# Optimization experiments

Hardware: AMD Instinct MI355X
Metric: run time of the kernel (lower is better)

The kernel has to match this reference:

```python
import jax, jax.numpy as jnp
import numpy as np

CHUNK = 128  # chunk size for the chunked causal linear-attention scan
EPS = 1e-6


def _feature_map(x):
    # elu(x) + 1, matching torch.nn.functional.elu (alpha=1)
    return jax.nn.elu(x) + 1.0


def _causal_linear(Q, K, V):
    """Chunked causal linear attention.

    Q, K: [N, H, L, D], V: [N, H, L, Dv] (float32).
    Computes out[l] = Q[l] @ sum_{s<=l} K[s]^T V[s] without materializing
    the O(L*D*Dv) cumulative outer-product tensor.
    """
    N, H, L, D = Q.shape
    Dv = V.shape[-1]
    C = L // CHUNK
    # [C, N, H, T, D]
    qc = jnp.moveaxis(Q.reshape(N, H, C, CHUNK, D), 2, 0)
    kc = jnp.moveaxis(K.reshape(N, H, C, CHUNK, D), 2, 0)
    vc = jnp.moveaxis(V.reshape(N, H, C, CHUNK, Dv), 2, 0)
    tri = jnp.tril(jnp.ones((CHUNK, CHUNK), dtype=Q.dtype))  # causal mask within chunk

    def step(S, qkv):
        q, k, v = qkv  # [N, H, T, D], [N, H, T, D], [N, H, T, Dv]
        attn = jnp.einsum('nhtd,nhsd->nhts', q, k) * tri
        out = jnp.einsum('nhts,nhse->nhte', attn, v) \
            + jnp.einsum('nhtd,nhde->nhte', q, S)
        S = S + jnp.einsum('nhsd,nhse->nhde', k, v)
        return S, out

    S0 = jnp.zeros((N, H, D, Dv), dtype=Q.dtype)
    _, outs = jax.lax.scan(step, S0, (qc, kc, vc))  # outs: [C, N, H, T, Dv]
    return jnp.moveaxis(outs, 0, 2).reshape(N, H, L, Dv)


def setup_inputs() -> dict:
    key = jax.random.key(0)
    kq, kk, kv = jax.random.split(key, 3)
    shape = (4, 8192, 8, 64)  # [N, L, H, D]
    return {
        'queries': jax.random.normal(kq, shape, dtype=jnp.float32),
        'keys': jax.random.normal(kk, shape, dtype=jnp.float32),
        'values': jax.random.normal(kv, shape, dtype=jnp.float32),
    }


def reference(queries, keys, values):
    dtype = queries.dtype
    Q = _feature_map(queries)  # [N, L, H, D]
    K = _feature_map(keys)
    # normalizer: Z = 1 / (Q . cumsum_l(K) + eps), shape [N, L, H]
    Z = 1.0 / (jnp.einsum('nlhi,nlhi->nlh', Q, jnp.cumsum(K, axis=1)) + EPS)
    # numerator computed in float32 per original causal_linear
    Qf = jnp.transpose(Q, (0, 2, 1, 3)).astype(jnp.float32)
    Kf = jnp.transpose(K, (0, 2, 1, 3)).astype(jnp.float32)
    Vf = jnp.transpose(values, (0, 2, 1, 3)).astype(jnp.float32)
    Vn = _causal_linear(Qf, Kf, Vf)  # [N, H, L, Dv]
    Vn = jnp.transpose(Vn, (0, 2, 1, 3)).astype(dtype)  # [N, L, H, Dv]
    return Vn * Z[:, :, :, None]
```

## Files before the change

kernel.cpp:

```cpp
#include <hip/hip_runtime.h>
#include <math.h>

#define N_    4
#define L_    8192
#define H_    8
#define NH_   32
#define CHK   64
#define NSEG  32
#define SEGC  4
#define NC_   128
#define ROWF  512
#define EPSF  1e-6f

typedef __attribute__((ext_vector_type(8))) short bf16x8;
typedef __attribute__((ext_vector_type(4))) float f32x4;
typedef __attribute__((ext_vector_type(4))) unsigned short us4;

__device__ __forceinline__ float fmap(float x) { return x > 0.f ? x + 1.f : __expf(x); }

__device__ __forceinline__ unsigned short f2bf(float x) {
  unsigned u = __float_as_uint(x);
  u += 0x7FFFu + ((u >> 16) & 1u);
  return (unsigned short)(u >> 16);
}
__device__ __forceinline__ float bf2f(unsigned short u) {
  return __uint_as_float(((unsigned)u) << 16);
}

__device__ __forceinline__ int sidx(int row, int col) {
  return row * 64 + (col ^ ((row & 7) << 3));
}

__device__ __forceinline__ f32x4 MFMA(bf16x8 a, bf16x8 b, f32x4 c) {
  return __builtin_amdgcn_mfma_f32_16x16x32_bf16(a, b, c, 0, 0, 0);
}

__global__ __launch_bounds__(256) void k_seg_sums(const float* __restrict__ keys,
                                                  const float* __restrict__ values,
                                                  float* __restrict__ SegTot,
                                                  unsigned short* __restrict__ IntraPre,
                                                  float* __restrict__ KsegTot,
                                                  float* __restrict__ KintraPre) {
  __shared__ unsigned short Kt[64 * 64];
  __shared__ unsigned short Vt[64 * 64];
  __shared__ float kacc[64];
  const int bid = blockIdx.x;
  const int nh = bid / NSEG, seg = bid % NSEG;
  const int n = nh / H_, h = nh % H_;
  const int tid = threadIdx.x;
  const int lane = tid & 63;
  const int wv = tid >> 6;
  const int lane15 = lane & 15, lg = lane >> 4;
  const int arow = wv * 16 + lane15;

  if (tid < 64) kacc[tid] = 0.f;
  __syncthreads();

  f32x4 sAcc[4];
#pragma unroll
  for (int nt = 0; nt < 4; ++nt) sAcc[nt] = (f32x4){0.f, 0.f, 0.f, 0.f};

  for (int ci = 0; ci < SEGC; ++ci) {
    const int c = seg * SEGC + ci;
    const int l0 = c * CHK;
    float kpart = 0.f;
    {
      const int d = tid & 63, sg = tid >> 6;
      const size_t gbase = ((size_t)(n * L_ + l0)) * ROWF + h * 64 + d;
      for (int rep = 0; rep < 4; ++rep) {
        const int s0 = (sg * 4 + rep) * 4;
        us4 wk, wvv;
#pragma unroll
        for (int j = 0; j < 4; ++j) {
          const size_t g = gbase + (size_t)(s0 + j) * ROWF;
          const float kf = fmap(keys[g]);
          kpart += kf;
          wk[j] = f2bf(kf);
          wvv[j] = f2bf(values[g]);
        }
        *(us4*)&Kt[sidx(d, s0)] = wk;
        *(us4*)&Vt[sidx(d, s0)] = wvv;
      }
    }
    {
      unsigned short* ip = IntraPre + ((size_t)nh * NC_ + c) * 4096;
#pragma unroll
      for (int nt = 0; nt < 4; ++nt)
#pragma unroll
        for (int r = 0; r < 4; ++r)
          ip[(size_t)(wv * 16 + lg * 4 + r) * 64 + nt * 16 + lane15] = f2bf(sAcc[nt][r]);
    }
    if (tid < 64) KintraPre[((size_t)nh * NC_ + c) * 64 + tid] = kacc[tid];
    __syncthreads();

    atomicAdd(&kacc[tid & 63], kpart);

    const bf16x8 av0 = *(const bf16x8*)&Vt[sidx(arow, lg * 8)];
    const bf16x8 av1 = *(const bf16x8*)&Vt[sidx(arow, (lg + 4) * 8)];
#pragma unroll
    for (int nt = 0; nt < 4; ++nt) {
      const int brow = nt * 16 + lane15;
      sAcc[nt] = MFMA(av0, *(const bf16x8*)&Kt[sidx(brow, lg * 8)], sAcc[nt]);
      sAcc[nt] = MFMA(av1, *(const bf16x8*)&Kt[sidx(brow, (lg + 4) * 8)], sAcc[nt]);
    }
    __syncthreads();
  }

  float* Sg = SegTot + (size_t)bid * 4096;
#pragma unroll
  for (int nt = 0; nt < 4; ++nt)
#pragma unroll
    for (int r = 0; r < 4; ++r)
      Sg[(size_t)(wv * 16 + lg * 4 + r) * 64 + nt * 16 + lane15] = sAcc[nt][r];
  if (tid < 64) KsegTot[(size_t)bid * 64 + tid] = kacc[tid];
}

__global__ __launch_bounds__(256) void k_prefix(float* __restrict__ SegTot, float* __restrict__ KsegTot) {
  const int tid = threadIdx.x;
  if (blockIdx.x < 512) {
    const int gid = blockIdx.x * 256 + tid;
    const int nh = gid >> 12, de = gid & 4095;
    float* p = SegTot + (size_t)nh * NSEG * 4096 + de;
    float run = 0.f;
    for (int s = 0; s < NSEG; ++s) {
      const float x = p[(size_t)s * 4096];
      p[(size_t)s * 4096] = run;
      run += x;
    }
  } else {
    const int gid = (blockIdx.x - 512) * 256 + tid;
    const int nh = gid >> 6, d = gid & 63;
    float* p = KsegTot + (size_t)nh * NSEG * 64 + d;
    float run = 0.f;
    for (int s = 0; s < NSEG; ++s) {
      const float x = p[s * 64];
      p[s * 64] = run;
      run += x;
    }
  }
}

__global__ __launch_bounds__(256, 6) void k_output(const float* __restrict__ queries,
                                                   const float* __restrict__ keys,
                                                   const float* __restrict__ values,
                                                   const float* __restrict__ SegPre,
                                                   const unsigned short* __restrict__ IntraPre,
                                                   const float* __restrict__ KsegPre,
                                                   const float* __restrict__ KintraPre,
                                                   float* __restrict__ out) {
  __shared__ unsigned short Ks[64 * 64];
  __shared__ unsigned short Vt[64 * 64];
  __shared__ unsigned short St[64 * 64];
  __shared__ float kpre[64];
  __shared__ float zinv[64];

  const int bid = blockIdx.x;
  const int nh = bid / NC_, c = bid % NC_;
  const int seg = c / SEGC;
  const int n = nh / H_, h = nh % H_;
  const int tid = threadIdx.x;
  const int lane = tid & 63;
  const int wv = tid >> 6;
  const int lane15 = lane & 15, lg = lane >> 4;
  const int t0w = wv * 16;
  const int trow = t0w + lane15;
  const int l0 = c * CHK;

  {
    const int r0 = tid >> 4, c4 = (tid & 15) * 4;
    for (int rep = 0; rep < 4; ++rep) {
      const int row = r0 + rep * 16;
      const size_t g = ((size_t)(n * L_ + l0 + row)) * ROWF + h * 64 + c4;
      const float4 k = *(const float4*)&keys[g];
      us4 uk;
      uk[0] = f2bf(fmap(k.x)); uk[1] = f2bf(fmap(k.y));
      uk[2] = f2bf(fmap(k.z)); uk[3] = f2bf(fmap(k.w));
      *(us4*)&Ks[sidx(row, c4)] = uk;
    }
  }
  {
    const int d = tid & 63, sg = tid >> 6;
    const size_t gbase = ((size_t)(n * L_ + l0)) * ROWF + h * 64 + d;
    for (int rep = 0; rep < 4; ++rep) {
      const int s0 = (sg * 4 + rep) * 4;
      us4 w;
#pragma unroll
      for (int j = 0; j < 4; ++j) w[j] = f2bf(values[gbase + (size_t)(s0 + j) * ROWF]);
      *(us4*)&Vt[sidx(d, s0)] = w;
    }
  }
  {
    const float* sp = SegPre + ((size_t)nh * NSEG + seg) * 4096;
    const unsigned short* ip = IntraPre + ((size_t)nh * NC_ + c) * 4096;
    const int r0 = tid >> 4, c4 = (tid & 15) * 4;
    for (int rep = 0; rep < 4; ++rep) {
      const int row = r0 + rep * 16;
      const float4 s4 = *(const float4*)&sp[row * 64 + c4];
      const us4 i4 = *(const us4*)&ip[row * 64 + c4];
      us4 w;
      w[0] = f2bf(s4.x + bf2f(i4[0]));
      w[1] = f2bf(s4.y + bf2f(i4[1]));
      w[2] = f2bf(s4.z + bf2f(i4[2]));
      w[3] = f2bf(s4.w + bf2f(i4[3]));
      *(us4*)&St[sidx(row, c4)] = w;
    }
  }
  if (tid < 64)
    kpre[tid] = KsegPre[((size_t)nh * NSEG + seg) * 64 + tid] +
                KintraPre[((size_t)nh * NC_ + c) * 64 + tid];
  bf16x8 qf0, qf1;
  {
    const size_t qg = ((size_t)(n * L_ + l0 + trow)) * ROWF + h * 64;
    const float4 a = *(const float4*)&queries[qg + lg * 8];
    const float4 b = *(const float4*)&queries[qg + lg * 8 + 4];
    const float4 cc = *(const float4*)&queries[qg + 32 + lg * 8];
    const float4 d4 = *(const float4*)&queries[qg + 32 + lg * 8 + 4];
    qf0[0] = (short)f2bf(fmap(a.x)); qf0[1] = (short)f2bf(fmap(a.y));
    qf0[2] = (short)f2bf(fmap(a.z)); qf0[3] = (short)f2bf(fmap(a.w));
    qf0[4] = (short)f2bf(fmap(b.x)); qf0[5] = (short)f2bf(fmap(b.y));
    qf0[6] = (short)f2bf(fmap(b.z)); qf0[7] = (short)f2bf(fmap(b.w));
    qf1[0] = (short)f2bf(fmap(cc.x)); qf1[1] = (short)f2bf(fmap(cc.y));
    qf1[2] = (short)f2bf(fmap(cc.z)); qf1[3] = (short)f2bf(fmap(cc.w));
    qf1[4] = (short)f2bf(fmap(d4.x)); qf1[5] = (short)f2bf(fmap(d4.y));
    qf1[6] = (short)f2bf(fmap(d4.z)); qf1[7] = (short)f2bf(fmap(d4.w));
  }
  __syncthreads();

  f32x4 aT[4];
#pragma unroll
  for (int nt = 0; nt < 4; ++nt) {
    const int srow = nt * 16 + lane15;
    f32x4 a = {0.f, 0.f, 0.f, 0.f};
    a = MFMA(*(const bf16x8*)&Ks[sidx(srow, lg * 8)], qf0, a);
    a = MFMA(*(const bf16x8*)&Ks[sidx(srow, (lg + 4) * 8)], qf1, a);
    aT[nt] = a;
  }
  float zp = 0.f;
#pragma unroll
  for (int j = 0; j < 8; ++j) zp += bf2f((unsigned short)qf0[j]) * kpre[lg * 8 + j];
#pragma unroll
  for (int j = 0; j < 8; ++j) zp += bf2f((unsigned short)qf1[j]) * kpre[32 + lg * 8 + j];

  __syncthreads();

  float rs = 0.f;
#pragma unroll
  for (int nt = 0; nt < 4; ++nt) {
    us4 w;
#pragma unroll
    for (int r = 0; r < 4; ++r) {
      const int s = nt * 16 + lg * 4 + r;
      const float v = (s <= trow) ? aT[nt][r] : 0.f;
      rs += v;
      w[r] = f2bf(v);
    }
    *(us4*)&Ks[sidx(trow, nt * 16 + lg * 4)] = w;
  }
  float den = rs + zp;
  den += __shfl_xor(den, 16);
  den += __shfl_xor(den, 32);
  const float zv = 1.f / (den + EPSF);
  if (lg == 0) zinv[trow] = zv;

  const bf16x8 af0 = *(const bf16x8*)&Ks[sidx(trow, lg * 8)];
  const bf16x8 af1 = *(const bf16x8*)&Ks[sidx(trow, 32 + lg * 8)];
#pragma unroll
  for (int nt = 0; nt < 4; ++nt) {
    const int brow = nt * 16 + lane15;
    f32x4 o = {0.f, 0.f, 0.f, 0.f};
    o = MFMA(af0, *(const bf16x8*)&Vt[sidx(brow, lg * 8)], o);
    o = MFMA(af1, *(const bf16x8*)&Vt[sidx(brow, (lg + 4) * 8)], o);
    o = MFMA(qf0, *(const bf16x8*)&St[sidx(brow, lg * 8)], o);
    o = MFMA(qf1, *(const bf16x8*)&St[sidx(brow, (lg + 4) * 8)], o);
    const int e = nt * 16 + lane15;
#pragma unroll
    for (int r = 0; r < 4; ++r) {
      const int t = t0w + lg * 4 + r;
      out[((size_t)(n * L_ + l0 + t)) * ROWF + h * 64 + e] = o[r] * zinv[t];
    }
  }
}

extern "C" void kernel_launch(void* const* d_in, const int* in_sizes, int n_in,
                              void* d_out, int out_size, void* d_ws, size_t ws_size,
                              hipStream_t stream) {
  const float* queries = (const float*)d_in[0];
  const float* keys    = (const float*)d_in[1];
  const float* values  = (const float*)d_in[2];
  float* out = (float*)d_out;

  const size_t segtot_e = (size_t)NH_ * NSEG * 4096;
  const size_t intra_e  = (size_t)NH_ * NC_ * 4096;
  const size_t kseg_e   = (size_t)NH_ * NSEG * 64;
  const size_t kintra_e = (size_t)NH_ * NC_ * 64;
  const size_t need = segtot_e * 4 + intra_e * 2 + kseg_e * 4 + kintra_e * 4;
  if (ws_size < need) return;
  float* SegTot = (float*)d_ws;
  unsigned short* IntraPre = (unsigned short*)(SegTot + segtot_e);
  float* KsegTot = (float*)(IntraPre + intra_e);
  float* KintraPre = KsegTot + kseg_e;

  hipLaunchKernelGGL(k_seg_sums, dim3(NH_ * NSEG), dim3(256), 0, stream,
                     keys, values, SegTot, IntraPre, KsegTot, KintraPre);
  hipLaunchKernelGGL(k_prefix, dim3(512 + 8), dim3(256), 0, stream, SegTot, KsegTot);
  hipLaunchKernelGGL(k_output, dim3(NH_ * NC_), dim3(256), 0, stream,
                     queries, keys, values, SegTot, IntraPre, KsegTot, KintraPre, out);
}
```

Measured before the change: 101.2 us.

## Vectorize global loads/stores and transpose MFMA outputs for contiguous writes

Global reads of keys and values now use float4 loads along the feature dimension, with the transpose into LDS done by scattered 16-bit stores. Column sums of keys are reduced with wave shuffles before a few LDS atomics, replacing one atomic per thread. MFMA operands are swapped so each lane holds four contiguous output columns, which allows float4 stores of the output and SegTot and us4 stores of IntraPre, and removes the zinv shared array. The output kernel also remaps block indices in a strided order to spread work across heads and chunks. The scalar LDS transpose writes may cause bank conflicts.

```diff
diff --git a/kernel.cpp b/kernel.cpp
--- a/kernel.cpp
+++ b/kernel.cpp
@@ -60,58 +60,71 @@
 #pragma unroll
   for (int nt = 0; nt < 4; ++nt) sAcc[nt] = (f32x4){0.f, 0.f, 0.f, 0.f};
 
+  const int d4 = tid >> 4, sg = tid & 15;
+
   for (int ci = 0; ci < SEGC; ++ci) {
     const int c = seg * SEGC + ci;
     const int l0 = c * CHK;
-    float kpart = 0.f;
-    {
-      const int d = tid & 63, sg = tid >> 6;
-      const size_t gbase = ((size_t)(n * L_ + l0)) * ROWF + h * 64 + d;
-      for (int rep = 0; rep < 4; ++rep) {
-        const int s0 = (sg * 4 + rep) * 4;
-        us4 wk, wvv;
-#pragma unroll
-        for (int j = 0; j < 4; ++j) {
-          const size_t g = gbase + (size_t)(s0 + j) * ROWF;
-          const float kf = fmap(keys[g]);
-          kpart += kf;
-          wk[j] = f2bf(kf);
-          wvv[j] = f2bf(values[g]);
-        }
-        *(us4*)&Kt[sidx(d, s0)] = wk;
-        *(us4*)&Vt[sidx(d, s0)] = wvv;
+    float kp[4] = {0.f, 0.f, 0.f, 0.f};
+#pragma unroll
+    for (int j = 0; j < 4; ++j) {
+      const int s = sg * 4 + j;
+      const size_t g = ((size_t)(n * L_ + l0 + s)) * ROWF + h * 64 + d4 * 4;
+      const float4 k4 = *(const float4*)&keys[g];
+      const float4 v4 = *(const float4*)&values[g];
+      const float kf[4] = {fmap(k4.x), fmap(k4.y), fmap(k4.z), fmap(k4.w)};
+      const float vf[4] = {v4.x, v4.y, v4.z, v4.w};
+#pragma unroll
+      for (int m = 0; m < 4; ++m) {
+        kp[m] += kf[m];
+        Kt[sidx(d4 * 4 + m, s)] = f2bf(kf[m]);
+        Vt[sidx(d4 * 4 + m, s)] = f2bf(vf[m]);
       }
     }
     {
       unsigned short* ip = IntraPre + ((size_t)nh * NC_ + c) * 4096;
-#pragma unroll
-      for (int nt = 0; nt < 4; ++nt)
-#pragma unroll
-        for (int r = 0; r < 4; ++r)
-          ip[(size_t)(wv * 16 + lg * 4 + r) * 64 + nt * 16 + lane15] = f2bf(sAcc[nt][r]);
+      const int e = wv * 16 + lane15;
+#pragma unroll
+      for (int nt = 0; nt < 4; ++nt) {
+        us4 w;
+#pragma unroll
+        for (int r = 0; r < 4; ++r) w[r] = f2bf(sAcc[nt][r]);
+        *(us4*)&ip[(size_t)e * 64 + nt * 16 + lg * 4] = w;
+      }
     }
     if (tid < 64) KintraPre[((size_t)nh * NC_ + c) * 64 + tid] = kacc[tid];
     __syncthreads();
 
-    atomicAdd(&kacc[tid & 63], kpart);
+#pragma unroll
+    for (int m = 0; m < 4; ++m) {
+      float v = kp[m];
+      v += __shfl_xor(v, 1);
+      v += __shfl_xor(v, 2);
+      v += __shfl_xor(v, 4);
+      v += __shfl_xor(v, 8);
+      if (lane15 == 0) atomicAdd(&kacc[d4 * 4 + m], v);
+    }
 
     const bf16x8 av0 = *(const bf16x8*)&Vt[sidx(arow, lg * 8)];
     const bf16x8 av1 = *(const bf16x8*)&Vt[sidx(arow, (lg + 4) * 8)];
 #pragma unroll
     for (int nt = 0; nt < 4; ++nt) {
       const int brow = nt * 16 + lane15;
-      sAcc[nt] = MFMA(av0, *(const bf16x8*)&Kt[sidx(brow, lg * 8)], sAcc[nt]);
-      sAcc[nt] = MFMA(av1, *(const bf16x8*)&Kt[sidx(brow, (lg + 4) * 8)], sAcc[nt]);
+      sAcc[nt] = MFMA(*(const bf16x8*)&Kt[sidx(brow, lg * 8)], av0, sAcc[nt]);
+      sAcc[nt] = MFMA(*(const bf16x8*)&Kt[sidx(brow, (lg + 4) * 8)], av1, sAcc[nt]);
     }
     __syncthreads();
   }
 
-  float* Sg = SegTot + (size_t)bid * 4096;
-#pragma unroll
-  for (int nt = 0; nt < 4; ++nt)
-#pragma unroll
-    for (int r = 0; r < 4; ++r)
-      Sg[(size_t)(wv * 16 + lg * 4 + r) * 64 + nt * 16 + lane15] = sAcc[nt][r];
+  {
+    float* Sg = SegTot + (size_t)bid * 4096;
+    const int e = wv * 16 + lane15;
+#pragma unroll
+    for (int nt = 0; nt < 4; ++nt) {
+      const float4 w = make_float4(sAcc[nt][0], sAcc[nt][1], sAcc[nt][2], sAcc[nt][3]);
+      *(float4*)&Sg[(size_t)e * 64 + nt * 16 + lg * 4] = w;
+    }
+  }
   if (tid < 64) KsegTot[(size_t)bid * 64 + tid] = kacc[tid];
 }
 
@@ -152,9 +165,9 @@
   __shared__ unsigned short Vt[64 * 64];
   __shared__ unsigned short St[64 * 64];
   __shared__ float kpre[64];
-  __shared__ float zinv[64];
-
-  const int bid = blockIdx.x;
+
+  const int wg = blockIdx.x;
+  const int bid = (wg & 7) * (NH_ * NC_ / 8) + (wg >> 3);
   const int nh = bid / NC_, c = bid % NC_;
   const int seg = c / SEGC;
   const int n = nh / H_, h = nh % H_;
@@ -179,14 +192,14 @@
     }
   }
   {
-    const int d = tid & 63, sg = tid >> 6;
-    const size_t gbase = ((size_t)(n * L_ + l0)) * ROWF + h * 64 + d;
-    for (int rep = 0; rep < 4; ++rep) {
-      const int s0 = (sg * 4 + rep) * 4;
-      us4 w;
-#pragma unroll
-      for (int j = 0; j < 4; ++j) w[j] = f2bf(values[gbase + (size_t)(s0 + j) * ROWF]);
-      *(us4*)&Vt[sidx(d, s0)] = w;
+    const int d4 = tid >> 4, sg = tid & 15;
+#pragma unroll
+    for (int j = 0; j < 4; ++j) {
+      const int s = sg * 4 + j;
+      const float4 v4 = *(const float4*)&values[((size_t)(n * L_ + l0 + s)) * ROWF + h * 64 + d4 * 4];
+      const float vf[4] = {v4.x, v4.y, v4.z, v4.w};
+#pragma unroll
+      for (int m = 0; m < 4; ++m) Vt[sidx(d4 * 4 + m, s)] = f2bf(vf[m]);
     }
   }
   {
@@ -260,24 +273,20 @@
   den += __shfl_xor(den, 16);
   den += __shfl_xor(den, 32);
   const float zv = 1.f / (den + EPSF);
-  if (lg == 0) zinv[trow] = zv;
 
   const bf16x8 af0 = *(const bf16x8*)&Ks[sidx(trow, lg * 8)];
   const bf16x8 af1 = *(const bf16x8*)&Ks[sidx(trow, 32 + lg * 8)];
+  const size_t obase = ((size_t)(n * L_ + l0 + trow)) * ROWF + h * 64;
 #pragma unroll
   for (int nt = 0; nt < 4; ++nt) {
     const int brow = nt * 16 + lane15;
     f32x4 o = {0.f, 0.f, 0.f, 0.f};
-    o = MFMA(af0, *(const bf16x8*)&Vt[sidx(brow, lg * 8)], o);
-    o = MFMA(af1, *(const bf16x8*)&Vt[sidx(brow, (lg + 4) * 8)], o);
-    o = MFMA(qf0, *(const bf16x8*)&St[sidx(brow, lg * 8)], o);
-    o = MFMA(qf1, *(const bf16x8*)&St[sidx(brow, (lg + 4) * 8)], o);
-    const int e = nt * 16 + lane15;
-#pragma unroll
-    for (int r = 0; r < 4; ++r) {
-      const int t = t0w + lg * 4 + r;
-      out[((size_t)(n * L_ + l0 + t)) * ROWF + h * 64 + e] = o[r] * zinv[t];
-    }
+    o = MFMA(*(const bf16x8*)&Vt[sidx(brow, lg * 8)], af0, o);
+    o = MFMA(*(const bf16x8*)&Vt[sidx(brow, (lg + 4) * 8)], af1, o);
+    o = MFMA(*(const bf16x8*)&St[sidx(brow, lg * 8)], qf0, o);
+    o = MFMA(*(const bf16x8*)&St[sidx(brow, (lg + 4) * 8)], qf1, o);
+    const float4 w = make_float4(o[0] * zv, o[1] * zv, o[2] * zv, o[3] * zv);
+    *(float4*)&out[obase + nt * 16 + lg * 4] = w;
   }
 }
 
```

New measurement: 105.1 us. 1.04x slower.

## Replace segment sums with per-chunk totals and full chunk-level bf16 scan

Applied to the files above, without the earlier changes.

The first kernel now runs one block per chunk (4096 blocks) instead of looping over 4 chunks per segment (1024 blocks). It writes a bf16 K^T V total and a key sum for each chunk, and the scan kernel turns these into exclusive prefixes across all 128 chunks in place. The output kernel then loads a ready bf16 state with no segment+intra combine, swaps MFMA operand order so it can store float4 rows and drop the zinv shared array, and remaps block IDs for L2 locality. The scan now accumulates in fp32 but reads and writes bf16 for every chunk, which adds rounding of the chunk totals and a longer serial scan loop in exchange for more parallelism in the first pass.

```diff
diff --git a/kernel.cpp b/kernel.cpp
--- a/kernel.cpp
+++ b/kernel.cpp
@@ -6,8 +6,6 @@
 #define H_    8
 #define NH_   32
 #define CHK   64
-#define NSEG  32
-#define SEGC  4
 #define NC_   128
 #define ROWF  512
 #define EPSF  1e-6f
@@ -35,17 +33,15 @@
   return __builtin_amdgcn_mfma_f32_16x16x32_bf16(a, b, c, 0, 0, 0);
 }
 
-__global__ __launch_bounds__(256) void k_seg_sums(const float* __restrict__ keys,
-                                                  const float* __restrict__ values,
-                                                  float* __restrict__ SegTot,
-                                                  unsigned short* __restrict__ IntraPre,
-                                                  float* __restrict__ KsegTot,
-                                                  float* __restrict__ KintraPre) {
+__global__ __launch_bounds__(256) void k_chunk_tot(const float* __restrict__ keys,
+                                                   const float* __restrict__ values,
+                                                   unsigned short* __restrict__ Tws,
+                                                   float* __restrict__ Kcs) {
   __shared__ unsigned short Kt[64 * 64];
   __shared__ unsigned short Vt[64 * 64];
   __shared__ float kacc[64];
   const int bid = blockIdx.x;
-  const int nh = bid / NSEG, seg = bid % NSEG;
+  const int nh = bid / NC_, c = bid % NC_;
   const int n = nh / H_, h = nh % H_;
   const int tid = threadIdx.x;
   const int lane = tid & 63;
@@ -54,88 +50,82 @@
   const int arow = wv * 16 + lane15;
 
   if (tid < 64) kacc[tid] = 0.f;
-  __syncthreads();
-
-  f32x4 sAcc[4];
-#pragma unroll
-  for (int nt = 0; nt < 4; ++nt) sAcc[nt] = (f32x4){0.f, 0.f, 0.f, 0.f};
-
-  for (int ci = 0; ci < SEGC; ++ci) {
-    const int c = seg * SEGC + ci;
-    const int l0 = c * CHK;
-    float kpart = 0.f;
-    {
-      const int d = tid & 63, sg = tid >> 6;
-      const size_t gbase = ((size_t)(n * L_ + l0)) * ROWF + h * 64 + d;
-      for (int rep = 0; rep < 4; ++rep) {
-        const int s0 = (sg * 4 + rep) * 4;
-        us4 wk, wvv;
-#pragma unroll
-        for (int j = 0; j < 4; ++j) {
-          const size_t g = gbase + (size_t)(s0 + j) * ROWF;
-          const float kf = fmap(keys[g]);
-          kpart += kf;
-          wk[j] = f2bf(kf);
-          wvv[j] = f2bf(values[g]);
-        }
-        *(us4*)&Kt[sidx(d, s0)] = wk;
-        *(us4*)&Vt[sidx(d, s0)] = wvv;
+
+  float kpart = 0.f;
+  {
+    const int d = tid & 63, sg = tid >> 6;
+    const size_t gbase = ((size_t)(n * L_ + c * CHK)) * ROWF + h * 64 + d;
+    for (int rep = 0; rep < 4; ++rep) {
+      const int s0 = (sg * 4 + rep) * 4;
+      us4 wk, wvv;
+#pragma unroll
+      for (int j = 0; j < 4; ++j) {
+        const size_t g = gbase + (size_t)(s0 + j) * ROWF;
+        const float kf = fmap(keys[g]);
+        kpart += kf;
+        wk[j] = f2bf(kf);
+        wvv[j] = f2bf(values[g]);
       }
-    }
-    {
-      unsigned short* ip = IntraPre + ((size_t)nh * NC_ + c) * 4096;
-#pragma unroll
-      for (int nt = 0; nt < 4; ++nt)
-#pragma unroll
-        for (int r = 0; r < 4; ++r)
-          ip[(size_t)(wv * 16 + lg * 4 + r) * 64 + nt * 16 + lane15] = f2bf(sAcc[nt][r]);
-    }
-    if (tid < 64) KintraPre[((size_t)nh * NC_ + c) * 64 + tid] = kacc[tid];
-    __syncthreads();
-
-    atomicAdd(&kacc[tid & 63], kpart);
-
-    const bf16x8 av0 = *(const bf16x8*)&Vt[sidx(arow, lg * 8)];
-    const bf16x8 av1 = *(const bf16x8*)&Vt[sidx(arow, (lg + 4) * 8)];
-#pragma unroll
-    for (int nt = 0; nt < 4; ++nt) {
-      const int brow = nt * 16 + lane15;
-      sAcc[nt] = MFMA(av0, *(const bf16x8*)&Kt[sidx(brow, lg * 8)], sAcc[nt]);
-      sAcc[nt] = MFMA(av1, *(const bf16x8*)&Kt[sidx(brow, (lg + 4) * 8)], sAcc[nt]);
-    }
-    __syncthreads();
-  }
-
-  float* Sg = SegTot + (size_t)bid * 4096;
-#pragma unroll
-  for (int nt = 0; nt < 4; ++nt)
-#pragma unroll
-    for (int r = 0; r < 4; ++r)
-      Sg[(size_t)(wv * 16 + lg * 4 + r) * 64 + nt * 16 + lane15] = sAcc[nt][r];
-  if (tid < 64) KsegTot[(size_t)bid * 64 + tid] = kacc[tid];
-}
-
-__global__ __launch_bounds__(256) void k_prefix(float* __restrict__ SegTot, float* __restrict__ KsegTot) {
+      *(us4*)&Kt[sidx(d, s0)] = wk;
+      *(us4*)&Vt[sidx(d, s0)] = wvv;
+    }
+  }
+  __syncthreads();
+
+  atomicAdd(&kacc[tid & 63], kpart);
+
+  const bf16x8 av0 = *(const bf16x8*)&Vt[sidx(arow, lg * 8)];
+  const bf16x8 av1 = *(const bf16x8*)&Vt[sidx(arow, (lg + 4) * 8)];
+  unsigned short* Tp = Tws + (size_t)bid * 4096;
+#pragma unroll
+  for (int nt = 0; nt < 4; ++nt) {
+    const int brow = nt * 16 + lane15;
+    f32x4 acc = {0.f, 0.f, 0.f, 0.f};
+    acc = MFMA(*(const bf16x8*)&Kt[sidx(brow, lg * 8)], av0, acc);
+    acc = MFMA(*(const bf16x8*)&Kt[sidx(brow, (lg + 4) * 8)], av1, acc);
+    us4 w;
+#pragma unroll
+    for (int r = 0; r < 4; ++r) w[r] = f2bf(acc[r]);
+    *(us4*)&Tp[(size_t)arow * 64 + nt * 16 + lg * 4] = w;
+  }
+  __syncthreads();
+  if (tid < 64) Kcs[(size_t)bid * 64 + tid] = kacc[tid];
+}
+
+__global__ __launch_bounds__(256) void k_scan(unsigned short* __restrict__ Tws,
+                                              float* __restrict__ Kcs) {
   const int tid = threadIdx.x;
   if (blockIdx.x < 512) {
     const int gid = blockIdx.x * 256 + tid;
     const int nh = gid >> 12, de = gid & 4095;
-    float* p = SegTot + (size_t)nh * NSEG * 4096 + de;
+    unsigned short* p = Tws + (size_t)nh * NC_ * 4096 + de;
     float run = 0.f;
-    for (int s = 0; s < NSEG; ++s) {
-      const float x = p[(size_t)s * 4096];
-      p[(size_t)s * 4096] = run;
-      run += x;
+    for (int s = 0; s < 32; ++s) {
+      const float x0 = bf2f(p[(size_t)(s * 4 + 0) * 4096]);
+      const float x1 = bf2f(p[(size_t)(s * 4 + 1) * 4096]);
+      const float x2 = bf2f(p[(size_t)(s * 4 + 2) * 4096]);
+      const float x3 = bf2f(p[(size_t)(s * 4 + 3) * 4096]);
+      p[(size_t)(s * 4 + 0) * 4096] = f2bf(run);
+      p[(size_t)(s * 4 + 1) * 4096] = f2bf(run + x0);
+      p[(size_t)(s * 4 + 2) * 4096] = f2bf(run + x0 + x1);
+      p[(size_t)(s * 4 + 3) * 4096] = f2bf(run + x0 + x1 + x2);
+      run += x0 + x1 + x2 + x3;
     }
   } else {
     const int gid = (blockIdx.x - 512) * 256 + tid;
     const int nh = gid >> 6, d = gid & 63;
-    float* p = KsegTot + (size_t)nh * NSEG * 64 + d;
+    float* p = Kcs + (size_t)nh * NC_ * 64 + d;
     float run = 0.f;
-    for (int s = 0; s < NSEG; ++s) {
-      const float x = p[s * 64];
-      p[s * 64] = run;
-      run += x;
+    for (int s = 0; s < 32; ++s) {
+      const float x0 = p[(size_t)(s * 4 + 0) * 64];
+      const float x1 = p[(size_t)(s * 4 + 1) * 64];
+      const float x2 = p[(size_t)(s * 4 + 2) * 64];
+      const float x3 = p[(size_t)(s * 4 + 3) * 64];
+      p[(size_t)(s * 4 + 0) * 64] = run;
+      p[(size_t)(s * 4 + 1) * 64] = run + x0;
+      p[(size_t)(s * 4 + 2) * 64] = run + x0 + x1;
+      p[(size_t)(s * 4 + 3) * 64] = run + x0 + x1 + x2;
+      run += x0 + x1 + x2 + x3;
     }
   }
 }
@@ -143,20 +133,17 @@
 __global__ __launch_bounds__(256, 6) void k_output(const float* __restrict__ queries,
                                                    const float* __restrict__ keys,
                                                    const float* __restrict__ values,
-                                                   const float* __restrict__ SegPre,
-                                                   const unsigned short* __restrict__ IntraPre,
-                                                   const float* __restrict__ KsegPre,
-                                                   const float* __restrict__ KintraPre,
+                                                   const unsigned short* __restrict__ Pws,
+                                                   const float* __restrict__ Kpre,
                                                    float* __restrict__ out) {
   __shared__ unsigned short Ks[64 * 64];
   __shared__ unsigned short Vt[64 * 64];
   __shared__ unsigned short St[64 * 64];
   __shared__ float kpre[64];
-  __shared__ float zinv[64];
-
-  const int bid = blockIdx.x;
+
+  const int wg = blockIdx.x;
+  const int bid = (wg & 7) * (NH_ * NC_ / 8) + (wg >> 3);
   const int nh = bid / NC_, c = bid % NC_;
-  const int seg = c / SEGC;
   const int n = nh / H_, h = nh % H_;
   const int tid = threadIdx.x;
   const int lane = tid & 63;
@@ -190,24 +177,14 @@
     }
   }
   {
-    const float* sp = SegPre + ((size_t)nh * NSEG + seg) * 4096;
-    const unsigned short* ip = IntraPre + ((size_t)nh * NC_ + c) * 4096;
+    const unsigned short* pp = Pws + (size_t)bid * 4096;
     const int r0 = tid >> 4, c4 = (tid & 15) * 4;
     for (int rep = 0; rep < 4; ++rep) {
       const int row = r0 + rep * 16;
-      const float4 s4 = *(const float4*)&sp[row * 64 + c4];
-      const us4 i4 = *(const us4*)&ip[row * 64 + c4];
-      us4 w;
-      w[0] = f2bf(s4.x + bf2f(i4[0]));
-      w[1] = f2bf(s4.y + bf2f(i4[1]));
-      w[2] = f2bf(s4.z + bf2f(i4[2]));
-      w[3] = f2bf(s4.w + bf2f(i4[3]));
-      *(us4*)&St[sidx(row, c4)] = w;
-    }
-  }
-  if (tid < 64)
-    kpre[tid] = KsegPre[((size_t)nh * NSEG + seg) * 64 + tid] +
-                KintraPre[((size_t)nh * NC_ + c) * 64 + tid];
+      *(us4*)&St[sidx(row, c4)] = *(const us4*)&pp[row * 64 + c4];
+    }
+  }
+  if (tid < 64) kpre[tid] = Kpre[(size_t)bid * 64 + tid];
   bf16x8 qf0, qf1;
   {
     const size_t qg = ((size_t)(n * L_ + l0 + trow)) * ROWF + h * 64;
@@ -260,24 +237,20 @@
   den += __shfl_xor(den, 16);
   den += __shfl_xor(den, 32);
   const float zv = 1.f / (den + EPSF);
-  if (lg == 0) zinv[trow] = zv;
 
   const bf16x8 af0 = *(const bf16x8*)&Ks[sidx(trow, lg * 8)];
   const bf16x8 af1 = *(const bf16x8*)&Ks[sidx(trow, 32 + lg * 8)];
+  const size_t obase = ((size_t)(n * L_ + l0 + trow)) * ROWF + h * 64;
 #pragma unroll
   for (int nt = 0; nt < 4; ++nt) {
     const int brow = nt * 16 + lane15;
     f32x4 o = {0.f, 0.f, 0.f, 0.f};
-    o = MFMA(af0, *(const bf16x8*)&Vt[sidx(brow, lg * 8)], o);
-    o = MFMA(af1, *(const bf16x8*)&Vt[sidx(brow, (lg + 4) * 8)], o);
-    o = MFMA(qf0, *(const bf16x8*)&St[sidx(brow, lg * 8)], o);
-    o = MFMA(qf1, *(const bf16x8*)&St[sidx(brow, (lg + 4) * 8)], o);
-    const int e = nt * 16 + lane15;
-#pragma unroll
-    for (int r = 0; r < 4; ++r) {
-      const int t = t0w + lg * 4 + r;
-      out[((size_t)(n * L_ + l0 + t)) * ROWF + h * 64 + e] = o[r] * zinv[t];
-    }
+    o = MFMA(*(const bf16x8*)&Vt[sidx(brow, lg * 8)], af0, o);
+    o = MFMA(*(const bf16x8*)&Vt[sidx(brow, (lg + 4) * 8)], af1, o);
+    o = MFMA(*(const bf16x8*)&St[sidx(brow, lg * 8)], qf0, o);
+    o = MFMA(*(const bf16x8*)&St[sidx(brow, (lg + 4) * 8)], qf1, o);
+    const float4 w = make_float4(o[0] * zv, o[1] * zv, o[2] * zv, o[3] * zv);
+    *(float4*)&out[obase + nt * 16 + lg * 4] = w;
   }
 }
 
@@ -289,20 +262,14 @@
   const float* values  = (const float*)d_in[2];
   float* out = (float*)d_out;
 
-  const size_t segtot_e = (size_t)NH_ * NSEG * 4096;
-  const size_t intra_e  = (size_t)NH_ * NC_ * 4096;
-  const size_t kseg_e   = (size_t)NH_ * NSEG * 64;
-  const size_t kintra_e = (size_t)NH_ * NC_ * 64;
-  const size_t need = segtot_e * 4 + intra_e * 2 + kseg_e * 4 + kintra_e * 4;
-  if (ws_size < need) return;
-  float* SegTot = (float*)d_ws;
-  unsigned short* IntraPre = (unsigned short*)(SegTot + segtot_e);
-  float* KsegTot = (float*)(IntraPre + intra_e);
-  float* KintraPre = KsegTot + kseg_e;
-
-  hipLaunchKernelGGL(k_seg_sums, dim3(NH_ * NSEG), dim3(256), 0, stream,
-                     keys, values, SegTot, IntraPre, KsegTot, KintraPre);
-  hipLaunchKernelGGL(k_prefix, dim3(512 + 8), dim3(256), 0, stream, SegTot, KsegTot);
+  const size_t t_elems = (size_t)NH_ * NC_ * 4096;
+  const size_t k_elems = (size_t)NH_ * NC_ * 64;
+  if (ws_size < t_elems * 2 + k_elems * 4) return;
+  unsigned short* Tws = (unsigned short*)d_ws;
+  float* Kcs = (float*)(Tws + t_elems);
+
+  hipLaunchKernelGGL(k_chunk_tot, dim3(NH_ * NC_), dim3(256), 0, stream, keys, values, Tws, Kcs);
+  hipLaunchKernelGGL(k_scan, dim3(512 + 8), dim3(256), 0, stream, Tws, Kcs);
   hipLaunchKernelGGL(k_output, dim3(NH_ * NC_), dim3(256), 0, stream,
-                     queries, keys, values, SegTot, IntraPre, KsegTot, KintraPre, out);
-}
+                     queries, keys, values, Tws, Kcs, out);
+}
```

New measurement: 96.21 us. 1.05x faster.
